# Kernel optimization log

Measured on AMD Instinct MI355X. Metric: run time of the kernel, lower is better.

Reference implementation:

```python
import jax, jax.numpy as jnp
import numpy as np

HEADS = 8
KD = 64  # key_dim
VD = 64  # value_dim


def _conv1x1(W, b, x):
    # 1x1 conv == per-pixel matmul over channels. W: [out, in], x: [b, in, h, w]
    return jnp.einsum('oc,bchw->bohw', W, x) + b[:, None, None]


def setup_inputs() -> dict:
    key = jax.random.key(0)
    ks = jax.random.split(key, 9)
    B, C, H, W = 4, 128, 128, 128
    s = 0.02
    return {
        'x':  jax.random.normal(ks[0], (B, C, H, W), jnp.float32),
        'Wq': jax.random.normal(ks[1], (KD * HEADS, C), jnp.float32) * s,
        'bq': jax.random.normal(ks[2], (KD * HEADS,), jnp.float32) * s,
        'Wk': jax.random.normal(ks[3], (KD * HEADS, C), jnp.float32) * s,
        'bk': jax.random.normal(ks[4], (KD * HEADS,), jnp.float32) * s,
        'Wv': jax.random.normal(ks[5], (VD * HEADS, C), jnp.float32) * s,
        'bv': jax.random.normal(ks[6], (VD * HEADS,), jnp.float32) * s,
        'Wo': jax.random.normal(ks[7], (C, VD * HEADS), jnp.float32) * s,
        'bo': jax.random.normal(ks[8], (C,), jnp.float32) * s,
    }


def reference(x, Wq, bq, Wk, bk, Wv, bv, Wo, bo):
    B, C, H, W = x.shape
    n = H * W
    scale = KD ** -0.25
    # projections -> [b, heads, dim, n]
    q = _conv1x1(Wq, bq, x).reshape(B, HEADS, KD, n) * scale
    k = _conv1x1(Wk, bk, x).reshape(B, HEADS, KD, n) * scale
    v = _conv1x1(Wv, bv, x).reshape(B, HEADS, VD, n)
    # linear attention: softmax k over tokens (n), softmax q over key dim (d)
    k = jax.nn.softmax(k, axis=-1)
    q = jax.nn.softmax(q, axis=-2)
    ctx = jnp.einsum('bhdn,bhen->bhde', k, v)   # [b, h, kd, vd] small context
    out = jnp.einsum('bhdn,bhde->bhen', q, ctx)  # [b, h, vd, n]
    out = out.reshape(B, HEADS * VD, H, W)
    return _conv1x1(Wo, bo, out)
```

## Files before the change

kernel.cpp:

```cpp
#include <hip/hip_runtime.h>

typedef unsigned short u16;
typedef __bf16 bf16x8 __attribute__((ext_vector_type(8)));
typedef float f32x4 __attribute__((ext_vector_type(4)));

#define N_ 16384
#define SCALE 0.35355339059327379f

__device__ __forceinline__ u16 f2bf(float f){
  union { float f; unsigned int i; } v; v.f = f;
  unsigned int b = v.i;
  return (u16)((b + 0x7FFFu + ((b >> 16) & 1u)) >> 16);
}
__device__ __forceinline__ unsigned int pack2bf(float a, float b){
  return ((unsigned int)f2bf(b) << 16) | (unsigned int)f2bf(a);
}

__global__ __launch_bounds__(256) void prep(const float* __restrict__ Wq,
    const float* __restrict__ bq, const float* __restrict__ Wk,
    const float* __restrict__ bk, const float* __restrict__ Wv,
    const float* __restrict__ bv, u16* __restrict__ wkvf, u16* __restrict__ wqf,
    float* __restrict__ bkv, float* __restrict__ bqs){
  const int T = blockIdx.x * 256 + threadIdx.x;
  if (T < 1024){
    int jj = T & 127, h = T >> 7;
    bkv[T] = (jj < 64) ? SCALE * bk[h * 64 + jj] : bv[h * 64 + jj - 64];
  } else if (T < 1536){
    bqs[T - 1024] = SCALE * bq[T - 1024];
  }
  const float* src; float sc; u16* dst;
  if (T < 16384){
    int l = T & 63, f = T >> 6;
    int ks = f & 3, jt = (f >> 2) & 7, h = f >> 5;
    int jj = 16 * jt + (l & 15);
    int k0 = ks * 32 + (l >> 4) * 8;
    if (jj < 64){ src = Wk + (size_t)(h * 64 + jj) * 128 + k0; sc = SCALE; }
    else        { src = Wv + (size_t)(h * 64 + jj - 64) * 128 + k0; sc = 1.f; }
    dst = wkvf + (size_t)f * 512 + l * 8;
  } else {
    int T2 = T - 16384;
    int l = T2 & 63, f = T2 >> 6;
    int ks = f & 3, dt = (f >> 2) & 3, h = f >> 4;
    int d = 16 * dt + (l & 15);
    int k0 = ks * 32 + (l >> 4) * 8;
    src = Wq + (size_t)(h * 64 + d) * 128 + k0; sc = SCALE;
    dst = wqf + (size_t)f * 512 + l * 8;
  }
  float4 a = *(const float4*)src, c = *(const float4*)(src + 4);
  ushort4 o0, o1;
  o0.x = f2bf(sc * a.x); o0.y = f2bf(sc * a.y); o0.z = f2bf(sc * a.z); o0.w = f2bf(sc * a.w);
  o1.x = f2bf(sc * c.x); o1.y = f2bf(sc * c.y); o1.z = f2bf(sc * c.z); o1.w = f2bf(sc * c.w);
  *(ushort4*)dst = o0; *(ushort4*)(dst + 4) = o1;
}

__global__ __launch_bounds__(256) void convx(const float* __restrict__ x,
                                             u16* __restrict__ xt){
  const int tid = threadIdx.x;
  const int b = blockIdx.y;
  const int kq = tid >> 6;
  const int t0 = blockIdx.x * 128 + 2 * (tid & 63);
  const float* xp = x + (size_t)(b * 128 + kq * 32) * N_ + t0;
  u16* dst = xt + (size_t)(b * N_ + t0) * 128;
#pragma unroll
  for (int gi = 0; gi < 4; gi++){
    float2 v[8];
#pragma unroll
    for (int j = 0; j < 8; j++)
      v[j] = *(const float2*)(xp + (size_t)(gi * 8 + j) * N_);
    const int g = kq * 4 + gi;
    {
      uint4 o;
      o.x = pack2bf(v[0].x, v[1].x); o.y = pack2bf(v[2].x, v[3].x);
      o.z = pack2bf(v[4].x, v[5].x); o.w = pack2bf(v[6].x, v[7].x);
      *(uint4*)(dst + ((g ^ (t0 & 15)) * 8)) = o;
    }
    {
      uint4 o;
      o.x = pack2bf(v[0].y, v[1].y); o.y = pack2bf(v[2].y, v[3].y);
      o.z = pack2bf(v[4].y, v[5].y); o.w = pack2bf(v[6].y, v[7].y);
      const int t = t0 + 1;
      *(uint4*)(dst + 128 + ((g ^ (t & 15)) * 8)) = o;
    }
  }
}

__global__ __launch_bounds__(256, 2) void kvctx(const u16* __restrict__ xt,
    const u16* __restrict__ wkvf, const float* __restrict__ bkv,
    float* __restrict__ pctx, float* __restrict__ prs){
  __shared__ u16 smem[32768];
  const int tid = threadIdx.x;
  const int chunk = blockIdx.x, h = blockIdx.y, b = blockIdx.z;
  const int w = tid >> 6, l = tid & 63, r15 = l & 15, q = l >> 4;
  const int th = w & 1, jh = w >> 1;

  bf16x8 wf[4][4];
#pragma unroll
  for (int ni = 0; ni < 4; ni++)
#pragma unroll
    for (int ks = 0; ks < 4; ks++)
      wf[ni][ks] = *(const bf16x8*)(wkvf +
          (size_t)((h * 8 + 4 * jh + ni) * 4 + ks) * 512 + l * 8);
  float barr[4];
#pragma unroll
  for (int ni = 0; ni < 4; ni++)
    barr[ni] = bkv[h * 128 + jh * 64 + 16 * ni + r15];

  const size_t tok0 = (size_t)b * N_ + chunk * 512;
  const char* gbase = (const char*)(xt + tok0 * 128);
  u16* sekv = smem + 16384;

#define STAGE(sub_)                                                            \
  {                                                                            \
    const char* gs = gbase + (size_t)(sub_)*32768 + w * 8192 + l * 16;         \
    char* ls = (char*)smem + w * 8192;                                         \
    _Pragma("unroll")                                                          \
    for (int p = 0; p < 8; p++)                                                \
      __builtin_amdgcn_global_load_lds(                                        \
          (const __attribute__((address_space(1))) void*)(gs + p * 1024),      \
          (__attribute__((address_space(3))) void*)(ls + p * 1024), 16, 0, 0); \
  }

  STAGE(0);
  __syncthreads();

  f32x4 acc2[4][4] = {};
  float rs[4] = {0.f, 0.f, 0.f, 0.f};

  for (int sub = 0; sub < 4; sub++){
    f32x4 acc1[4][4] = {};
#pragma unroll
    for (int ks = 0; ks < 4; ks++){
      bf16x8 xa[4];
#pragma unroll
      for (int mi = 0; mi < 4; mi++){
        int t = th * 64 + 16 * mi + r15;
        xa[mi] = *(const bf16x8*)&smem[t * 128 + (((ks * 4 + q) ^ r15) * 8)];
      }
#pragma unroll
      for (int mi = 0; mi < 4; mi++)
#pragma unroll
        for (int ni = 0; ni < 4; ni++)
          acc1[mi][ni] = __builtin_amdgcn_mfma_f32_16x16x32_bf16(
              xa[mi], wf[ni][ks], acc1[mi][ni], 0, 0, 0);
    }
#pragma unroll
    for (int ni = 0; ni < 4; ni++){
      const float bb = barr[ni];
      const int j = jh * 64 + 16 * ni + r15;
      float ps = 0.f;
#pragma unroll
      for (int mi = 0; mi < 4; mi++){
        float vals[4];
#pragma unroll
        for (int r = 0; r < 4; r++) vals[r] = acc1[mi][ni][r] + bb;
        if (jh == 0){
#pragma unroll
          for (int r = 0; r < 4; r++){ vals[r] = __expf(vals[r]); ps += vals[r]; }
        }
        uint2 pk;
        pk.x = pack2bf(vals[0], vals[1]);
        pk.y = pack2bf(vals[2], vals[3]);
        int g8 = 16 * th + 4 * mi + q;
        int g8s = g8 ^ (2 * r15);
        *(uint2*)&sekv[j * 128 + g8s * 4] = pk;
      }
      if (jh == 0){
        ps += __shfl_xor(ps, 16); ps += __shfl_xor(ps, 32);
        rs[ni] += ps;
      }
    }
    __syncthreads();
    if (sub < 3) STAGE(sub + 1);
    {
      bf16x8 ka[4], va[4];
      const int g8s = (8 * w + 2 * q) ^ (2 * r15);
#pragma unroll
      for (int mi2 = 0; mi2 < 4; mi2++){
        int d = 16 * mi2 + r15;
        ka[mi2] = *(const bf16x8*)&sekv[d * 128 + g8s * 4];
      }
#pragma unroll
      for (int ni2 = 0; ni2 < 4; ni2++){
        int e = 16 * ni2 + r15;
        va[ni2] = *(const bf16x8*)&sekv[(64 + e) * 128 + g8s * 4];
      }
#pragma unroll
      for (int mi2 = 0; mi2 < 4; mi2++)
#pragma unroll
        for (int ni2 = 0; ni2 < 4; ni2++)
          acc2[mi2][ni2] = __builtin_amdgcn_mfma_f32_16x16x32_bf16(
              ka[mi2], va[ni2], acc2[mi2][ni2], 0, 0, 0);
    }
    __syncthreads();
  }
#undef STAGE
  float* fb = (float*)smem;
#pragma unroll
  for (int mi2 = 0; mi2 < 4; mi2++)
#pragma unroll
    for (int ni2 = 0; ni2 < 4; ni2++)
#pragma unroll
      for (int r = 0; r < 4; r++){
        int d = 16 * mi2 + 4 * q + r, e = 16 * ni2 + r15;
        fb[w * 4096 + d * 64 + e] = acc2[mi2][ni2][r];
      }
  __syncthreads();
  {
    float* dst = pctx + ((size_t)((b * 8 + h) * 32 + chunk)) * 4096 + tid * 16;
#pragma unroll
    for (int i = 0; i < 4; i++){
      int o = tid * 16 + 4 * i;
      float4 a = *(const float4*)(fb + o);
      float4 c = *(const float4*)(fb + 4096 + o);
      float4 d = *(const float4*)(fb + 8192 + o);
      float4 e = *(const float4*)(fb + 12288 + o);
      float4 s;
      s.x = a.x + c.x + d.x + e.x; s.y = a.y + c.y + d.y + e.y;
      s.z = a.z + c.z + d.z + e.z; s.w = a.w + c.w + d.w + e.w;
      *(float4*)(dst + 4 * i) = s;
    }
  }
  if (jh == 0 && q == 0){
    float* rb = prs + ((size_t)((b * 8 + h) * 32 + chunk)) * 128 + th * 64;
#pragma unroll
    for (int ni = 0; ni < 4; ni++) rb[16 * ni + r15] = rs[ni];
  }
}

__global__ __launch_bounds__(256) void ctxred(const float* __restrict__ pctx,
    const float* __restrict__ prs, float* __restrict__ ctx,
    float* __restrict__ rowsum){
  const int bh = blockIdx.x, s = blockIdx.y, tid = threadIdx.x;
  const float2* base = (const float2*)(pctx + (size_t)bh * 32 * 4096 + s * 512) + tid;
  float2 acc = {0.f, 0.f};
#pragma unroll 4
  for (int t = 0; t < 32; t++){
    float2 v = base[t * 2048];
    acc.x += v.x; acc.y += v.y;
  }
  *((float2*)(ctx + (size_t)bh * 4096 + s * 512) + tid) = acc;
  if (s == 0 && tid < 64){
    const float* rb = prs + (size_t)bh * 32 * 128 + tid;
    float sm = 0.f;
    for (int t = 0; t < 32; t++) sm += rb[t * 128] + rb[t * 128 + 64];
    rowsum[bh * 64 + tid] = sm;
  }
}

__global__ __launch_bounds__(256) void mker(const float* __restrict__ ctx,
    const float* __restrict__ Wo, const float* __restrict__ rowsum,
    u16* __restrict__ mtf){
  __shared__ float ctxh[64][68];
  __shared__ float woht[64][132];
  const int tid = threadIdx.x;
  const int h = blockIdx.x, b = blockIdx.y;
  const int bh = b * 8 + h;
  const int e4 = tid & 15, r0 = tid >> 4;
#pragma unroll
  for (int p = 0; p < 4; p++){
    int d = r0 + p * 16;
    float4 v = *(const float4*)(ctx + ((size_t)bh * 64 + d) * 64 + 4 * e4);
    *(float4*)&ctxh[d][4 * e4] = v;
  }
#pragma unroll
  for (int p = 0; p < 8; p++){
    int c = r0 + p * 16;
    float4 v = *(const float4*)(Wo + (size_t)c * 512 + h * 64 + 4 * e4);
    woht[4 * e4 + 0][c] = v.x; woht[4 * e4 + 1][c] = v.y;
    woht[4 * e4 + 2][c] = v.z; woht[4 * e4 + 3][c] = v.w;
  }
  __syncthreads();
  const int cg = tid & 3, d = tid >> 2;
  const float inv = 1.f / rowsum[bh * 64 + d];
  float acc[32];
#pragma unroll
  for (int cc = 0; cc < 32; cc++) acc[cc] = 0.f;
  for (int e = 0; e < 64; e++){
    float cv = ctxh[d][e];
#pragma unroll
    for (int cc = 0; cc < 32; cc++) acc[cc] += cv * woht[e][cg + 4 * cc];
  }
  const int ks = d >> 5, lq = ((d >> 3) & 3) << 4, el = d & 7;
#pragma unroll
  for (int cc = 0; cc < 32; cc++){
    int c = cg + 4 * cc;
    mtf[((size_t)(bh * 8 + (c >> 4)) * 2 + ks) * 512 + ((c & 15) | lq) * 8 + el]
        = f2bf(inv * acc[cc]);
  }
}

__global__ __launch_bounds__(256, 3) void qout(const u16* __restrict__ xt,
    const u16* __restrict__ wqf, const float* __restrict__ bqs,
    const u16* __restrict__ mtf, const float* __restrict__ bo,
    float* __restrict__ out){
  __shared__ u16 smP[4][16 * 64];
  const int tid = threadIdx.x;
  const int tt = blockIdx.x, b = blockIdx.y;
  const int w = tid >> 6, l = tid & 63, r15 = l & 15, q = l >> 4;
  const int t0 = tt * 64;
  const int m7 = 2 * (r15 & 7);
  const int t = t0 + w * 16 + r15;

  bf16x8 xb[4];
#pragma unroll
  for (int ks = 0; ks < 4; ks++)
    xb[ks] = *(const bf16x8*)(xt + (size_t)(b * N_ + t) * 128 +
                              (((ks * 4 + q) ^ r15) * 8));

  u16* sp = smP[w];
  f32x4 acc3[8] = {};
  for (int h = 0; h < 8; h++){
    float bq_[4][4];
#pragma unroll
    for (int mi = 0; mi < 4; mi++){
      float4 v = *(const float4*)(bqs + h * 64 + 16 * mi + 4 * q);
      bq_[mi][0] = v.x; bq_[mi][1] = v.y; bq_[mi][2] = v.z; bq_[mi][3] = v.w;
    }
    f32x4 acc1[4] = {};
#pragma unroll
    for (int ks = 0; ks < 4; ks++){
      bf16x8 wqv[4];
#pragma unroll
      for (int mi = 0; mi < 4; mi++)
        wqv[mi] = *(const bf16x8*)(wqf +
            (size_t)((h * 4 + mi) * 4 + ks) * 512 + l * 8);
#pragma unroll
      for (int mi = 0; mi < 4; mi++)
        acc1[mi] = __builtin_amdgcn_mfma_f32_16x16x32_bf16(
            wqv[mi], xb[ks], acc1[mi], 0, 0, 0);
    }
    {
      float ps = 0.f;
#pragma unroll
      for (int mi = 0; mi < 4; mi++)
#pragma unroll
        for (int r = 0; r < 4; r++){
          float e = __expf(acc1[mi][r] + bq_[mi][r]);
          acc1[mi][r] = e; ps += e;
        }
      ps += __shfl_xor(ps, 16); ps += __shfl_xor(ps, 32);
      const float ci = 1.f / ps;
#pragma unroll
      for (int mi = 0; mi < 4; mi++){
        uint2 pk;
        pk.x = pack2bf(acc1[mi][0] * ci, acc1[mi][1] * ci);
        pk.y = pack2bf(acc1[mi][2] * ci, acc1[mi][3] * ci);
        int g8s = (4 * mi + q) ^ m7;
        *(uint2*)&sp[r15 * 64 + g8s * 4] = pk;
      }
    }
#pragma unroll
    for (int ks2 = 0; ks2 < 2; ks2++){
      const int g8s = (8 * ks2 + 2 * q) ^ m7;
      bf16x8 pb = *(const bf16x8*)&sp[r15 * 64 + g8s * 4];
#pragma unroll
      for (int half = 0; half < 2; half++){
        bf16x8 mf[4];
#pragma unroll
        for (int mm = 0; mm < 4; mm++)
          mf[mm] = *(const bf16x8*)(mtf +
              ((size_t)((b * 8 + h) * 8 + half * 4 + mm) * 2 + ks2) * 512 + l * 8);
#pragma unroll
        for (int mm = 0; mm < 4; mm++)
          acc3[half * 4 + mm] = __builtin_amdgcn_mfma_f32_16x16x32_bf16(
              mf[mm], pb, acc3[half * 4 + mm], 0, 0, 0);
      }
    }
  }
#pragma unroll
  for (int mi = 0; mi < 8; mi++){
    float4 bv = *(const float4*)(bo + 16 * mi + 4 * q);
    float bs[4] = {bv.x, bv.y, bv.z, bv.w};
#pragma unroll
    for (int r = 0; r < 4; r++){
      int c = 16 * mi + 4 * q + r;
      out[(size_t)(b * 128 + c) * N_ + t] = acc3[mi][r] + bs[r];
    }
  }
}

extern "C" void kernel_launch(void* const* d_in, const int* in_sizes, int n_in,
                              void* d_out, int out_size, void* d_ws, size_t ws_size,
                              hipStream_t stream){
  const float* x  = (const float*)d_in[0];
  const float* Wq = (const float*)d_in[1];
  const float* bq = (const float*)d_in[2];
  const float* Wk = (const float*)d_in[3];
  const float* bk = (const float*)d_in[4];
  const float* Wv = (const float*)d_in[5];
  const float* bv = (const float*)d_in[6];
  const float* Wo = (const float*)d_in[7];
  const float* bo = (const float*)d_in[8];
  float* out = (float*)d_out;

  char* ws = (char*)d_ws;
  u16*   xt     = (u16*)ws;
  u16*   wkvf   = (u16*)(ws + 16777216);
  u16*   wqf    = (u16*)(ws + 17039360);
  u16*   mtf    = (u16*)(ws + 17170432);
  float* bkv    = (float*)(ws + 17694720);
  float* bqs    = (float*)(ws + 17698816);
  float* rowsum = (float*)(ws + 17700864);
  float* ctx    = (float*)(ws + 17709056);
  float* pctx   = (float*)(ws + 18233344);
  float* prs    = (float*)(ws + 35010560);

  prep <<<96, 256, 0, stream>>>(Wq, bq, Wk, bk, Wv, bv, wkvf, wqf, bkv, bqs);
  convx<<<dim3(128, 4), 256, 0, stream>>>(x, xt);
  kvctx<<<dim3(32, 8, 4), 256, 0, stream>>>(xt, wkvf, bkv, pctx, prs);
  ctxred<<<dim3(32, 8), 256, 0, stream>>>(pctx, prs, ctx, rowsum);
  mker <<<dim3(8, 4), 256, 0, stream>>>(ctx, Wo, rowsum, mtf);
  qout <<<dim3(256, 4), 256, 0, stream>>>(xt, wqf, bqs, mtf, bo, out);
}
```

Before: 202.8 us.

## Merge prep/convx and ctxred/mker kernels, use hardware bf16 convert, overlap staging

Folds the weight-prep and x-transpose kernels into one launch, and folds the context reduction and Wo-projection kernels into a single kernel spread over 256 blocks instead of 32. This cuts launches and removes the ctx/rowsum round trip. It swaps the software bf16 rounding for the v_cvt_pk_bf16_f32 instruction, which may round slightly differently. In kvctx the next-stage prefetch now starts right after the first MFMA phase behind an explicit barrier. In qout the mtf fragment loads are hoisted and software-pipelined ahead of the softmax.

After: 192.0 us. 1.06x faster.

```diff
diff --git a/kernel.cpp b/kernel.cpp
--- a/kernel.cpp
+++ b/kernel.cpp
@@ -12,16 +12,50 @@
   unsigned int b = v.i;
   return (u16)((b + 0x7FFFu + ((b >> 16) & 1u)) >> 16);
 }
-__device__ __forceinline__ unsigned int pack2bf(float a, float b){
-  return ((unsigned int)f2bf(b) << 16) | (unsigned int)f2bf(a);
-}
-
-__global__ __launch_bounds__(256) void prep(const float* __restrict__ Wq,
+__device__ __forceinline__ unsigned int cvtpk(float a, float b){
+  unsigned int r;
+  asm("v_cvt_pk_bf16_f32 %0, %1, %2" : "=v"(r) : "v"(a), "v"(b));
+  return r;
+}
+
+__global__ __launch_bounds__(256) void pconvx(const float* __restrict__ x,
+    u16* __restrict__ xt, const float* __restrict__ Wq,
     const float* __restrict__ bq, const float* __restrict__ Wk,
     const float* __restrict__ bk, const float* __restrict__ Wv,
     const float* __restrict__ bv, u16* __restrict__ wkvf, u16* __restrict__ wqf,
     float* __restrict__ bkv, float* __restrict__ bqs){
-  const int T = blockIdx.x * 256 + threadIdx.x;
+  const int tid = threadIdx.x;
+  const int bid = blockIdx.x;
+  if (bid < 512){
+    const int b = bid >> 7;
+    const int kq = tid >> 6;
+    const int t0 = (bid & 127) * 128 + 2 * (tid & 63);
+    const float* xp = x + (size_t)(b * 128 + kq * 32) * N_ + t0;
+    u16* dst = xt + (size_t)(b * N_ + t0) * 128;
+#pragma unroll
+    for (int gi = 0; gi < 4; gi++){
+      float2 v[8];
+#pragma unroll
+      for (int j = 0; j < 8; j++)
+        v[j] = *(const float2*)(xp + (size_t)(gi * 8 + j) * N_);
+      const int g = kq * 4 + gi;
+      {
+        uint4 o;
+        o.x = cvtpk(v[0].x, v[1].x); o.y = cvtpk(v[2].x, v[3].x);
+        o.z = cvtpk(v[4].x, v[5].x); o.w = cvtpk(v[6].x, v[7].x);
+        *(uint4*)(dst + ((g ^ (t0 & 15)) * 8)) = o;
+      }
+      {
+        uint4 o;
+        o.x = cvtpk(v[0].y, v[1].y); o.y = cvtpk(v[2].y, v[3].y);
+        o.z = cvtpk(v[4].y, v[5].y); o.w = cvtpk(v[6].y, v[7].y);
+        const int t = t0 + 1;
+        *(uint4*)(dst + 128 + ((g ^ (t & 15)) * 8)) = o;
+      }
+    }
+    return;
+  }
+  const int T = (bid - 512) * 256 + tid;
   if (T < 1024){
     int jj = T & 127, h = T >> 7;
     bkv[T] = (jj < 64) ? SCALE * bk[h * 64 + jj] : bv[h * 64 + jj - 64];
@@ -53,37 +87,6 @@
   *(ushort4*)dst = o0; *(ushort4*)(dst + 4) = o1;
 }
 
-__global__ __launch_bounds__(256) void convx(const float* __restrict__ x,
-                                             u16* __restrict__ xt){
-  const int tid = threadIdx.x;
-  const int b = blockIdx.y;
-  const int kq = tid >> 6;
-  const int t0 = blockIdx.x * 128 + 2 * (tid & 63);
-  const float* xp = x + (size_t)(b * 128 + kq * 32) * N_ + t0;
-  u16* dst = xt + (size_t)(b * N_ + t0) * 128;
-#pragma unroll
-  for (int gi = 0; gi < 4; gi++){
-    float2 v[8];
-#pragma unroll
-    for (int j = 0; j < 8; j++)
-      v[j] = *(const float2*)(xp + (size_t)(gi * 8 + j) * N_);
-    const int g = kq * 4 + gi;
-    {
-      uint4 o;
-      o.x = pack2bf(v[0].x, v[1].x); o.y = pack2bf(v[2].x, v[3].x);
-      o.z = pack2bf(v[4].x, v[5].x); o.w = pack2bf(v[6].x, v[7].x);
-      *(uint4*)(dst + ((g ^ (t0 & 15)) * 8)) = o;
-    }
-    {
-      uint4 o;
-      o.x = pack2bf(v[0].y, v[1].y); o.y = pack2bf(v[2].y, v[3].y);
-      o.z = pack2bf(v[4].y, v[5].y); o.w = pack2bf(v[6].y, v[7].y);
-      const int t = t0 + 1;
-      *(uint4*)(dst + 128 + ((g ^ (t & 15)) * 8)) = o;
-    }
-  }
-}
-
 __global__ __launch_bounds__(256, 2) void kvctx(const u16* __restrict__ xt,
     const u16* __restrict__ wkvf, const float* __restrict__ bkv,
     float* __restrict__ pctx, float* __restrict__ prs){
@@ -143,6 +146,9 @@
           acc1[mi][ni] = __builtin_amdgcn_mfma_f32_16x16x32_bf16(
               xa[mi], wf[ni][ks], acc1[mi][ni], 0, 0, 0);
     }
+    asm volatile("s_waitcnt lgkmcnt(0)" ::: "memory");
+    __builtin_amdgcn_s_barrier();
+    if (sub < 3) STAGE(sub + 1);
 #pragma unroll
     for (int ni = 0; ni < 4; ni++){
       const float bb = barr[ni];
@@ -158,8 +164,8 @@
           for (int r = 0; r < 4; r++){ vals[r] = __expf(vals[r]); ps += vals[r]; }
         }
         uint2 pk;
-        pk.x = pack2bf(vals[0], vals[1]);
-        pk.y = pack2bf(vals[2], vals[3]);
+        pk.x = cvtpk(vals[0], vals[1]);
+        pk.y = cvtpk(vals[2], vals[3]);
         int g8 = 16 * th + 4 * mi + q;
         int g8s = g8 ^ (2 * r15);
         *(uint2*)&sekv[j * 128 + g8s * 4] = pk;
@@ -169,8 +175,8 @@
         rs[ni] += ps;
       }
     }
-    __syncthreads();
-    if (sub < 3) STAGE(sub + 1);
+    asm volatile("s_waitcnt lgkmcnt(0)" ::: "memory");
+    __builtin_amdgcn_s_barrier();
     {
       bf16x8 ka[4], va[4];
       const int g8s = (8 * w + 2 * q) ^ (2 * r15);
@@ -227,65 +233,63 @@
   }
 }
 
-__global__ __launch_bounds__(256) void ctxred(const float* __restrict__ pctx,
-    const float* __restrict__ prs, float* __restrict__ ctx,
-    float* __restrict__ rowsum){
-  const int bh = blockIdx.x, s = blockIdx.y, tid = threadIdx.x;
-  const float2* base = (const float2*)(pctx + (size_t)bh * 32 * 4096 + s * 512) + tid;
-  float2 acc = {0.f, 0.f};
+__global__ __launch_bounds__(256) void redmker(const float* __restrict__ pctx,
+    const float* __restrict__ prs, const float* __restrict__ Wo,
+    u16* __restrict__ mtf){
+  __shared__ float ctxh8[8][68];
+  __shared__ float woht[64][132];
+  __shared__ float rsh[8];
+  const int tid = threadIdx.x;
+  const int bh = blockIdx.x, s = blockIdx.y;
+  const int h = bh & 7;
+  {
+    const int e4 = tid & 15, r0 = tid >> 4;
+#pragma unroll
+    for (int p = 0; p < 8; p++){
+      int c = r0 + p * 16;
+      float4 v = *(const float4*)(Wo + (size_t)c * 512 + h * 64 + 4 * e4);
+      woht[4 * e4 + 0][c] = v.x; woht[4 * e4 + 1][c] = v.y;
+      woht[4 * e4 + 2][c] = v.z; woht[4 * e4 + 3][c] = v.w;
+    }
+  }
+  {
+    const float* base = pctx + (size_t)bh * 131072 + s * 512 + tid * 2;
+    float2 a = {0.f, 0.f};
 #pragma unroll 4
-  for (int t = 0; t < 32; t++){
-    float2 v = base[t * 2048];
-    acc.x += v.x; acc.y += v.y;
-  }
-  *((float2*)(ctx + (size_t)bh * 4096 + s * 512) + tid) = acc;
-  if (s == 0 && tid < 64){
-    const float* rb = prs + (size_t)bh * 32 * 128 + tid;
-    float sm = 0.f;
-    for (int t = 0; t < 32; t++) sm += rb[t * 128] + rb[t * 128 + 64];
-    rowsum[bh * 64 + tid] = sm;
-  }
-}
-
-__global__ __launch_bounds__(256) void mker(const float* __restrict__ ctx,
-    const float* __restrict__ Wo, const float* __restrict__ rowsum,
-    u16* __restrict__ mtf){
-  __shared__ float ctxh[64][68];
-  __shared__ float woht[64][132];
-  const int tid = threadIdx.x;
-  const int h = blockIdx.x, b = blockIdx.y;
-  const int bh = b * 8 + h;
-  const int e4 = tid & 15, r0 = tid >> 4;
-#pragma unroll
-  for (int p = 0; p < 4; p++){
-    int d = r0 + p * 16;
-    float4 v = *(const float4*)(ctx + ((size_t)bh * 64 + d) * 64 + 4 * e4);
-    *(float4*)&ctxh[d][4 * e4] = v;
-  }
-#pragma unroll
-  for (int p = 0; p < 8; p++){
-    int c = r0 + p * 16;
-    float4 v = *(const float4*)(Wo + (size_t)c * 512 + h * 64 + 4 * e4);
-    woht[4 * e4 + 0][c] = v.x; woht[4 * e4 + 1][c] = v.y;
-    woht[4 * e4 + 2][c] = v.z; woht[4 * e4 + 3][c] = v.w;
+    for (int c = 0; c < 32; c++){
+      float2 v = *(const float2*)(base + c * 4096);
+      a.x += v.x; a.y += v.y;
+    }
+    const int i = tid * 2;
+    ctxh8[i >> 6][i & 63] = a.x;
+    ctxh8[(i + 1) >> 6][(i + 1) & 63] = a.y;
+  }
+  {
+    const int dl = tid >> 5, c = tid & 31;
+    const int dg = s * 8 + dl;
+    const float* rb = prs + (size_t)bh * 4096 + c * 128;
+    float v = rb[dg] + rb[64 + dg];
+    v += __shfl_xor(v, 1);  v += __shfl_xor(v, 2);
+    v += __shfl_xor(v, 4);  v += __shfl_xor(v, 8);
+    v += __shfl_xor(v, 16);
+    if (c == 0) rsh[dl] = v;
   }
   __syncthreads();
-  const int cg = tid & 3, d = tid >> 2;
-  const float inv = 1.f / rowsum[bh * 64 + d];
-  float acc[32];
-#pragma unroll
-  for (int cc = 0; cc < 32; cc++) acc[cc] = 0.f;
+  const int dl = tid >> 5, c0 = (tid & 31) * 4;
+  const int d = s * 8 + dl;
+  const float inv = 1.f / rsh[dl];
+  float acc[4] = {0.f, 0.f, 0.f, 0.f};
   for (int e = 0; e < 64; e++){
-    float cv = ctxh[d][e];
-#pragma unroll
-    for (int cc = 0; cc < 32; cc++) acc[cc] += cv * woht[e][cg + 4 * cc];
+    float cv = ctxh8[dl][e];
+#pragma unroll
+    for (int j = 0; j < 4; j++) acc[j] += cv * woht[e][c0 + j];
   }
   const int ks = d >> 5, lq = ((d >> 3) & 3) << 4, el = d & 7;
 #pragma unroll
-  for (int cc = 0; cc < 32; cc++){
-    int c = cg + 4 * cc;
+  for (int j = 0; j < 4; j++){
+    int c = c0 + j;
     mtf[((size_t)(bh * 8 + (c >> 4)) * 2 + ks) * 512 + ((c & 15) | lq) * 8 + el]
-        = f2bf(inv * acc[cc]);
+        = f2bf(inv * acc[j]);
   }
 }
 
@@ -329,6 +333,15 @@
         acc1[mi] = __builtin_amdgcn_mfma_f32_16x16x32_bf16(
             wqv[mi], xb[ks], acc1[mi], 0, 0, 0);
     }
+    bf16x8 mfA[4], mfB[4];
+#pragma unroll
+    for (int mm = 0; mm < 4; mm++)
+      mfA[mm] = *(const bf16x8*)(mtf +
+          ((size_t)((b * 8 + h) * 8 + mm) * 2 + 0) * 512 + l * 8);
+#pragma unroll
+    for (int mm = 0; mm < 4; mm++)
+      mfB[mm] = *(const bf16x8*)(mtf +
+          ((size_t)((b * 8 + h) * 8 + 4 + mm) * 2 + 0) * 512 + l * 8);
     {
       float ps = 0.f;
 #pragma unroll
@@ -343,29 +356,38 @@
 #pragma unroll
       for (int mi = 0; mi < 4; mi++){
         uint2 pk;
-        pk.x = pack2bf(acc1[mi][0] * ci, acc1[mi][1] * ci);
-        pk.y = pack2bf(acc1[mi][2] * ci, acc1[mi][3] * ci);
+        pk.x = cvtpk(acc1[mi][0] * ci, acc1[mi][1] * ci);
+        pk.y = cvtpk(acc1[mi][2] * ci, acc1[mi][3] * ci);
         int g8s = (4 * mi + q) ^ m7;
         *(uint2*)&sp[r15 * 64 + g8s * 4] = pk;
       }
     }
-#pragma unroll
-    for (int ks2 = 0; ks2 < 2; ks2++){
-      const int g8s = (8 * ks2 + 2 * q) ^ m7;
-      bf16x8 pb = *(const bf16x8*)&sp[r15 * 64 + g8s * 4];
-#pragma unroll
-      for (int half = 0; half < 2; half++){
-        bf16x8 mf[4];
-#pragma unroll
-        for (int mm = 0; mm < 4; mm++)
-          mf[mm] = *(const bf16x8*)(mtf +
-              ((size_t)((b * 8 + h) * 8 + half * 4 + mm) * 2 + ks2) * 512 + l * 8);
-#pragma unroll
-        for (int mm = 0; mm < 4; mm++)
-          acc3[half * 4 + mm] = __builtin_amdgcn_mfma_f32_16x16x32_bf16(
-              mf[mm], pb, acc3[half * 4 + mm], 0, 0, 0);
-      }
-    }
+    bf16x8 pb0 = *(const bf16x8*)&sp[r15 * 64 + (((2 * q) ^ m7) * 4)];
+    bf16x8 pb1 = *(const bf16x8*)&sp[r15 * 64 + (((8 + 2 * q) ^ m7) * 4)];
+#pragma unroll
+    for (int mm = 0; mm < 4; mm++)
+      acc3[mm] = __builtin_amdgcn_mfma_f32_16x16x32_bf16(
+          mfA[mm], pb0, acc3[mm], 0, 0, 0);
+#pragma unroll
+    for (int mm = 0; mm < 4; mm++)
+      mfA[mm] = *(const bf16x8*)(mtf +
+          ((size_t)((b * 8 + h) * 8 + mm) * 2 + 1) * 512 + l * 8);
+#pragma unroll
+    for (int mm = 0; mm < 4; mm++)
+      acc3[4 + mm] = __builtin_amdgcn_mfma_f32_16x16x32_bf16(
+          mfB[mm], pb0, acc3[4 + mm], 0, 0, 0);
+#pragma unroll
+    for (int mm = 0; mm < 4; mm++)
+      mfB[mm] = *(const bf16x8*)(mtf +
+          ((size_t)((b * 8 + h) * 8 + 4 + mm) * 2 + 1) * 512 + l * 8);
+#pragma unroll
+    for (int mm = 0; mm < 4; mm++)
+      acc3[mm] = __builtin_amdgcn_mfma_f32_16x16x32_bf16(
+          mfA[mm], pb1, acc3[mm], 0, 0, 0);
+#pragma unroll
+    for (int mm = 0; mm < 4; mm++)
+      acc3[4 + mm] = __builtin_amdgcn_mfma_f32_16x16x32_bf16(
+          mfB[mm], pb1, acc3[4 + mm], 0, 0, 0);
   }
 #pragma unroll
   for (int mi = 0; mi < 8; mi++){
@@ -400,15 +422,12 @@
   u16*   mtf    = (u16*)(ws + 17170432);
   float* bkv    = (float*)(ws + 17694720);
   float* bqs    = (float*)(ws + 17698816);
-  float* rowsum = (float*)(ws + 17700864);
-  float* ctx    = (float*)(ws + 17709056);
   float* pctx   = (float*)(ws + 18233344);
   float* prs    = (float*)(ws + 35010560);
 
-  prep <<<96, 256, 0, stream>>>(Wq, bq, Wk, bk, Wv, bv, wkvf, wqf, bkv, bqs);
-  convx<<<dim3(128, 4), 256, 0, stream>>>(x, xt);
-  kvctx<<<dim3(32, 8, 4), 256, 0, stream>>>(xt, wkvf, bkv, pctx, prs);
-  ctxred<<<dim3(32, 8), 256, 0, stream>>>(pctx, prs, ctx, rowsum);
-  mker <<<dim3(8, 4), 256, 0, stream>>>(ctx, Wo, rowsum, mtf);
-  qout <<<dim3(256, 4), 256, 0, stream>>>(xt, wqf, bqs, mtf, bo, out);
-}
+  pconvx <<<608, 256, 0, stream>>>(x, xt, Wq, bq, Wk, bk, Wv, bv,
+                                   wkvf, wqf, bkv, bqs);
+  kvctx  <<<dim3(32, 8, 4), 256, 0, stream>>>(xt, wkvf, bkv, pctx, prs);
+  redmker<<<dim3(32, 8), 256, 0, stream>>>(pctx, prs, Wo, mtf);
+  qout   <<<dim3(256, 4), 256, 0, stream>>>(xt, wqf, bqs, mtf, bo, out);
+}
```
